# Kernel tuning notes

Hardware: AMD Instinct MI355X
Metric: run time of the kernel (lower is better)

The kernel has to match this reference:

```python
import jax, jax.numpy as jnp
import numpy as np

LN_EPS = 1e-5


def setup_inputs() -> dict:
    key = jax.random.key(0)
    k1, k2, k3, k4, k5, k6 = jax.random.split(key, 6)
    B, S, P = 4, 4096, 16          # batch, seq_len, max_n_bytes
    LR, D = 256, 1024              # lowrank_dim, embedding_dim
    # byte ids in [-1, 255]; -1 marks missing bytes
    bytes_ids = jax.random.randint(k1, (B, S, P), -1, 256)
    byte_table = jax.random.normal(k2, (256, LR), dtype=jnp.float32) * 0.02
    pos_emb = jax.random.normal(k3, (P, LR, LR), dtype=jnp.float32)
    W_up = jax.random.normal(k4, (D, LR), dtype=jnp.float32) * 0.02
    b_up = jnp.zeros((D,), dtype=jnp.float32)
    ln_gamma = jnp.ones((D,), dtype=jnp.float32)
    ln_beta = jnp.zeros((D,), dtype=jnp.float32)
    return {
        "bytes_ids": bytes_ids,
        "byte_table": byte_table,
        "pos_emb": pos_emb,
        "W_up": W_up,
        "b_up": b_up,
        "ln_gamma": ln_gamma,
        "ln_beta": ln_beta,
    }


def reference(bytes_ids, byte_table, pos_emb, W_up, b_up, ln_gamma, ln_beta):
    # bytes_ids: [B, S, P] int, -1 => missing byte
    missing = bytes_ids == -1                             # [B,S,P]
    ids = jnp.where(missing, 0, bytes_ids)
    be = byte_table[ids]                                  # [B,S,P,LR] gather
    # per-position small matmul: pos_emb[p] applied to each byte embedding
    emb = jnp.einsum('pij,bspi->bspj', pos_emb, be)       # [B,S,P,LR]
    emb = jnp.where(missing[..., None], 0.0, emb)         # mask missing bytes
    emb = emb.sum(axis=-2)                                # [B,S,LR]
    x = emb @ W_up.T + b_up                               # [B,S,D]
    # layernorm
    mu = x.mean(axis=-1, keepdims=True)
    var = jnp.mean(jnp.square(x - mu), axis=-1, keepdims=True)
    return (x - mu) * jax.lax.rsqrt(var + LN_EPS) * ln_gamma + ln_beta
```

## Files before the change

kernel.cpp:

```cpp
#include <hip/hip_runtime.h>
#include <stdint.h>

#define PP     16
#define LRDIM  256
#define DDIM   1024
#define LN_EPS 1e-5f

typedef __attribute__((ext_vector_type(8))) short  short8;
typedef __attribute__((ext_vector_type(4))) float  f32x4;

__device__ __forceinline__ uint32_t bf16_rne(float f) {
    uint32_t u = __builtin_bit_cast(uint32_t, f);
    return (u + 0x7fffu + ((u >> 16) & 1u)) >> 16;
}
__device__ __forceinline__ float bf_lo(uint32_t u) {
    return __builtin_bit_cast(float, u << 16);
}
__device__ __forceinline__ float bf_hi(uint32_t u) {
    return __builtin_bit_cast(float, u & 0xffff0000u);
}

__global__ __launch_bounds__(256) void k_prep(const float* __restrict__ bt,
                                              const float* __restrict__ pe,
                                              const float* __restrict__ W,
                                              unsigned short* __restrict__ t2b,
                                              uint4* __restrict__ wb) {
    if (blockIdx.x < 512) {
        const int p  = blockIdx.x >> 5;
        const int c0 = (blockIdx.x & 31) << 3;
        const int j  = threadIdx.x;
        const float* pep = pe + (size_t)p * LRDIM * LRDIM;
        float a[8];
#pragma unroll
        for (int r = 0; r < 8; ++r) a[r] = 0.f;
#pragma unroll 4
        for (int i = 0; i < LRDIM; ++i) {
            const float v = pep[i * LRDIM + j];
#pragma unroll
            for (int r = 0; r < 8; ++r)
                a[r] = fmaf(v, bt[(c0 + r) * LRDIM + i], a[r]);
        }
#pragma unroll
        for (int r = 0; r < 8; ++r)
            t2b[(size_t)((p << 8) + c0 + r) * LRDIM + j] =
                (unsigned short)bf16_rne(a[r]);
    } else {
        const int gt  = (blockIdx.x - 512) * 256 + threadIdx.x;
        const int l   = gt & 63;
        const int ks  = (gt >> 6) & 7;
        const int nfg = gt >> 9;
        const int n   = nfg * 16 + (l & 15);
        const int k   = ks * 32 + (l >> 4) * 8;
        const float* src = W + (size_t)n * LRDIM + k;
        uint32_t r[4];
#pragma unroll
        for (int q = 0; q < 4; ++q) {
            const uint32_t lo = bf16_rne(src[2 * q + 0]);
            const uint32_t hi = bf16_rne(src[2 * q + 1]);
            r[q] = lo | (hi << 16);
        }
        wb[gt] = make_uint4(r[0], r[1], r[2], r[3]);
    }
}

__global__ __launch_bounds__(256) void k_gather(const int* __restrict__ ids,
                                                const unsigned short* __restrict__ t2b,
                                                uint2* __restrict__ Aq,
                                                int ntok) {
    const int wid = (blockIdx.x << 2) + (threadIdx.x >> 6);
    const int l   = threadIdx.x & 63;
    if (wid >= ntok) return;

    const int myid = (l < PP) ? ids[(size_t)wid * PP + l] : -1;

    float a0 = 0.f, a1 = 0.f, a2 = 0.f, a3 = 0.f;
#pragma unroll
    for (int p = 0; p < PP; ++p) {
        const int   id  = __shfl(myid, p);
        const float msk = (id >= 0) ? 1.f : 0.f;
        const uint2 v = *(const uint2*)(t2b +
                          ((size_t)((p << 8) + (id & 255)) << 8) + (l << 2));
        a0 = fmaf(msk, bf_lo(v.x), a0);
        a1 = fmaf(msk, bf_hi(v.x), a1);
        a2 = fmaf(msk, bf_lo(v.y), a2);
        a3 = fmaf(msk, bf_hi(v.y), a3);
    }
    uint2 pk;
    pk.x = bf16_rne(a0) | (bf16_rne(a1) << 16);
    pk.y = bf16_rne(a2) | (bf16_rne(a3) << 16);
    Aq[(size_t)wid * 64 + l] = pk;
}

__global__ __launch_bounds__(512, 4) void k_gemm(const unsigned short* __restrict__ A,
                                                 const uint4* __restrict__ wb,
                                                 const float* __restrict__ b_up,
                                                 const float* __restrict__ gamma,
                                                 const float* __restrict__ beta,
                                                 float* __restrict__ out,
                                                 int ntok) {
    __shared__ float ln_s[8][32];
    __shared__ float ln_ss[8][32];

    const int t    = threadIdx.x;
    const int w    = t >> 6;
    const int l    = t & 63;
    const int lo4  = l & 15;
    const int hi2  = l >> 4;
    const int tok0 = blockIdx.x << 5;

    f32x4 acc[2][8];
#pragma unroll
    for (int m2 = 0; m2 < 2; ++m2)
#pragma unroll
        for (int nf = 0; nf < 8; ++nf) {
            f32x4 z = {0.f, 0.f, 0.f, 0.f};
            acc[m2][nf] = z;
        }

    const unsigned short* Abase = A + ((size_t)tok0 << 8);

#pragma unroll
    for (int ks = 0; ks < 8; ++ks) {
        short8 af[2];
#pragma unroll
        for (int m2 = 0; m2 < 2; ++m2) {
            const int row = (m2 << 4) + lo4;
            af[m2] = *(const short8*)(Abase + ((size_t)row << 8) + (ks << 5) + (hi2 << 3));
        }
#pragma unroll
        for (int nf = 0; nf < 8; ++nf) {
            const int nfg = (w << 3) + nf;
            const uint4 bv = wb[(size_t)((nfg << 3) + ks) * 64 + l];
            const short8 bfr = __builtin_bit_cast(short8, bv);
            acc[0][nf] = __builtin_amdgcn_mfma_f32_16x16x32_bf16(af[0], bfr, acc[0][nf], 0, 0, 0);
            acc[1][nf] = __builtin_amdgcn_mfma_f32_16x16x32_bf16(af[1], bfr, acc[1][nf], 0, 0, 0);
        }
    }

    float s_[8], ss_[8];
#pragma unroll
    for (int q = 0; q < 8; ++q) { s_[q] = 0.f; ss_[q] = 0.f; }

#pragma unroll
    for (int nf = 0; nf < 8; ++nf) {
        const int col = (w << 7) + (nf << 4) + lo4;
        const float bu = b_up[col];
#pragma unroll
        for (int m2 = 0; m2 < 2; ++m2) {
            f32x4 v = acc[m2][nf];
            v.x += bu; v.y += bu; v.z += bu; v.w += bu;
            acc[m2][nf] = v;
            const int q0 = m2 * 4;
            s_[q0 + 0] += v.x; ss_[q0 + 0] += v.x * v.x;
            s_[q0 + 1] += v.y; ss_[q0 + 1] += v.y * v.y;
            s_[q0 + 2] += v.z; ss_[q0 + 2] += v.z * v.z;
            s_[q0 + 3] += v.w; ss_[q0 + 3] += v.w * v.w;
        }
    }
#pragma unroll
    for (int off = 1; off < 16; off <<= 1)
#pragma unroll
        for (int q = 0; q < 8; ++q) {
            s_[q]  += __shfl_xor(s_[q], off);
            ss_[q] += __shfl_xor(ss_[q], off);
        }
    if (lo4 == 0) {
#pragma unroll
        for (int q = 0; q < 8; ++q) {
            const int tl = (q >> 2) * 16 + hi2 * 4 + (q & 3);
            ln_s[w][tl]  = s_[q];
            ln_ss[w][tl] = ss_[q];
        }
    }
    __syncthreads();

    float mu_[8], inv_[8];
#pragma unroll
    for (int q = 0; q < 8; ++q) {
        const int tl = (q >> 2) * 16 + hi2 * 4 + (q & 3);
        float S = 0.f, SS = 0.f;
#pragma unroll
        for (int ww = 0; ww < 8; ++ww) { S += ln_s[ww][tl]; SS += ln_ss[ww][tl]; }
        const float mu  = S * (1.f / DDIM);
        const float var = SS * (1.f / DDIM) - mu * mu;
        mu_[q]  = mu;
        inv_[q] = rsqrtf(var + LN_EPS);
    }

#pragma unroll
    for (int nf = 0; nf < 8; ++nf) {
        const int col = (w << 7) + (nf << 4) + lo4;
        const float g  = gamma[col];
        const float bb = beta[col];
#pragma unroll
        for (int m2 = 0; m2 < 2; ++m2) {
            const f32x4 v = acc[m2][nf];
#pragma unroll
            for (int r = 0; r < 4; ++r) {
                const int q   = m2 * 4 + r;
                const int tl  = m2 * 16 + hi2 * 4 + r;
                const int tok = tok0 + tl;
                if (tok < ntok)
                    out[(size_t)tok * DDIM + col] = (v[r] - mu_[q]) * inv_[q] * g + bb;
            }
        }
    }
}

extern "C" void kernel_launch(void* const* d_in, const int* in_sizes, int n_in,
                              void* d_out, int out_size, void* d_ws, size_t ws_size,
                              hipStream_t stream) {
    const int*   ids   = (const int*)  d_in[0];
    const float* bt    = (const float*)d_in[1];
    const float* pe    = (const float*)d_in[2];
    const float* W     = (const float*)d_in[3];
    const float* b_up  = (const float*)d_in[4];
    const float* gamma = (const float*)d_in[5];
    const float* beta  = (const float*)d_in[6];
    float* out = (float*)d_out;

    const int ntok = in_sizes[0] / PP;

    char* ws = (char*)d_ws;
    unsigned short* t2b = (unsigned short*)(ws);
    uint4*          wbb = (uint4*)(ws + (2 << 20));
    unsigned short* Abf = (unsigned short*)(ws + (3 << 20));
    uint2*          Aq  = (uint2*)Abf;

    hipLaunchKernelGGL(k_prep, dim3(640), dim3(256), 0, stream, bt, pe, W, t2b, wbb);
    hipLaunchKernelGGL(k_gather, dim3((ntok + 3) / 4), dim3(256), 0, stream,
                       ids, t2b, Aq, ntok);
    hipLaunchKernelGGL(k_gemm, dim3((ntok + 31) / 32), dim3(512), 0, stream,
                       Abf, wbb, b_up, gamma, beta, out, ntok);
}
```

Baseline: 90.16 us.

## Restructure GEMM to 16-token tiles with LDS-staged A and double-buffered B

The GEMM+LayerNorm kernel now processes 16 tokens per block with 4 waves, each wave covering 256 output columns (16 MFMA tiles) instead of 32 tokens × 128 columns. The A tile is staged once into swizzled LDS to avoid bank conflicts, and the B fragments are software-pipelined with two register buffers so weight loads overlap the MFMAs. This halves A reuse per B fragment (B is reloaded per 16 tokens, so weight traffic from L2 doubles) in exchange for more blocks and latency hiding.

```diff
diff --git a/kernel.cpp b/kernel.cpp
--- a/kernel.cpp
+++ b/kernel.cpp
@@ -91,96 +91,122 @@
     Aq[(size_t)wid * 64 + l] = pk;
 }
 
-__global__ __launch_bounds__(512, 4) void k_gemm(const unsigned short* __restrict__ A,
+__global__ __launch_bounds__(256, 4) void k_gemm(const unsigned short* __restrict__ A,
                                                  const uint4* __restrict__ wb,
                                                  const float* __restrict__ b_up,
                                                  const float* __restrict__ gamma,
                                                  const float* __restrict__ beta,
                                                  float* __restrict__ out,
                                                  int ntok) {
-    __shared__ float ln_s[8][32];
-    __shared__ float ln_ss[8][32];
+    __shared__ __align__(16) unsigned char As[16 * 512];
+    __shared__ float ln_s[4][16];
+    __shared__ float ln_ss[4][16];
 
     const int t    = threadIdx.x;
     const int w    = t >> 6;
     const int l    = t & 63;
     const int lo4  = l & 15;
     const int hi2  = l >> 4;
-    const int tok0 = blockIdx.x << 5;
-
-    f32x4 acc[2][8];
-#pragma unroll
-    for (int m2 = 0; m2 < 2; ++m2)
-#pragma unroll
-        for (int nf = 0; nf < 8; ++nf) {
-            f32x4 z = {0.f, 0.f, 0.f, 0.f};
-            acc[m2][nf] = z;
-        }
-
-    const unsigned short* Abase = A + ((size_t)tok0 << 8);
+    const int tok0 = blockIdx.x << 4;
+
+    {
+        const int r = t >> 4;
+        const int c = t & 15;
+        const uint4* asrc = (const uint4*)(A + ((size_t)(tok0 + r) << 8)) + (c << 1);
+        const uint4 v0 = asrc[0];
+        const uint4 v1 = asrc[1];
+        const int sw = (r & 7) << 4;
+        *(uint4*)(As + (r << 9) + (((c << 5)     ) ^ sw)) = v0;
+        *(uint4*)(As + (r << 9) + (((c << 5) + 16) ^ sw)) = v1;
+    }
+    __syncthreads();
+
+    f32x4 acc[16];
+#pragma unroll
+    for (int nf = 0; nf < 16; ++nf) {
+        f32x4 z = {0.f, 0.f, 0.f, 0.f};
+        acc[nf] = z;
+    }
+
+    const uint4* wp = wb + ((size_t)w << 13) + l;
+    const int swz = (lo4 & 7) << 4;
+
+    uint4 bA[4], bB[4];
+#pragma unroll
+    for (int h = 0; h < 4; ++h) bA[h] = wp[h * 512];
 
 #pragma unroll
     for (int ks = 0; ks < 8; ++ks) {
-        short8 af[2];
-#pragma unroll
-        for (int m2 = 0; m2 < 2; ++m2) {
-            const int row = (m2 << 4) + lo4;
-            af[m2] = *(const short8*)(Abase + ((size_t)row << 8) + (ks << 5) + (hi2 << 3));
-        }
-#pragma unroll
-        for (int nf = 0; nf < 8; ++nf) {
-            const int nfg = (w << 3) + nf;
-            const uint4 bv = wb[(size_t)((nfg << 3) + ks) * 64 + l];
-            const short8 bfr = __builtin_bit_cast(short8, bv);
-            acc[0][nf] = __builtin_amdgcn_mfma_f32_16x16x32_bf16(af[0], bfr, acc[0][nf], 0, 0, 0);
-            acc[1][nf] = __builtin_amdgcn_mfma_f32_16x16x32_bf16(af[1], bfr, acc[1][nf], 0, 0, 0);
-        }
-    }
-
-    float s_[8], ss_[8];
-#pragma unroll
-    for (int q = 0; q < 8; ++q) { s_[q] = 0.f; ss_[q] = 0.f; }
-
-#pragma unroll
-    for (int nf = 0; nf < 8; ++nf) {
-        const int col = (w << 7) + (nf << 4) + lo4;
+        const short8 af = *(const short8*)(As + (lo4 << 9) +
+                                           (((ks << 6) + (hi2 << 4)) ^ swz));
+#pragma unroll
+        for (int g = 0; g < 4; ++g) {
+            const int gn   = (g + 1) & 3;
+            const int kn   = (g == 3) ? ks + 1 : ks;
+            const bool last = (ks == 7) && (g == 3);
+            if ((g & 1) == 0) {
+                if (!last) {
+#pragma unroll
+                    for (int h = 0; h < 4; ++h)
+                        bB[h] = wp[(gn * 4 + h) * 512 + kn * 64];
+                }
+#pragma unroll
+                for (int h = 0; h < 4; ++h)
+                    acc[g * 4 + h] = __builtin_amdgcn_mfma_f32_16x16x32_bf16(
+                        af, __builtin_bit_cast(short8, bA[h]), acc[g * 4 + h], 0, 0, 0);
+            } else {
+                if (!last) {
+#pragma unroll
+                    for (int h = 0; h < 4; ++h)
+                        bA[h] = wp[(gn * 4 + h) * 512 + kn * 64];
+                }
+#pragma unroll
+                for (int h = 0; h < 4; ++h)
+                    acc[g * 4 + h] = __builtin_amdgcn_mfma_f32_16x16x32_bf16(
+                        af, __builtin_bit_cast(short8, bB[h]), acc[g * 4 + h], 0, 0, 0);
+            }
+        }
+    }
+
+    float s_[4], ss_[4];
+#pragma unroll
+    for (int q = 0; q < 4; ++q) { s_[q] = 0.f; ss_[q] = 0.f; }
+
+#pragma unroll
+    for (int nf = 0; nf < 16; ++nf) {
+        const int col = (w << 8) + (nf << 4) + lo4;
         const float bu = b_up[col];
-#pragma unroll
-        for (int m2 = 0; m2 < 2; ++m2) {
-            f32x4 v = acc[m2][nf];
-            v.x += bu; v.y += bu; v.z += bu; v.w += bu;
-            acc[m2][nf] = v;
-            const int q0 = m2 * 4;
-            s_[q0 + 0] += v.x; ss_[q0 + 0] += v.x * v.x;
-            s_[q0 + 1] += v.y; ss_[q0 + 1] += v.y * v.y;
-            s_[q0 + 2] += v.z; ss_[q0 + 2] += v.z * v.z;
-            s_[q0 + 3] += v.w; ss_[q0 + 3] += v.w * v.w;
-        }
+        f32x4 v = acc[nf];
+        v.x += bu; v.y += bu; v.z += bu; v.w += bu;
+        acc[nf] = v;
+        s_[0] += v.x; ss_[0] += v.x * v.x;
+        s_[1] += v.y; ss_[1] += v.y * v.y;
+        s_[2] += v.z; ss_[2] += v.z * v.z;
+        s_[3] += v.w; ss_[3] += v.w * v.w;
     }
 #pragma unroll
     for (int off = 1; off < 16; off <<= 1)
 #pragma unroll
-        for (int q = 0; q < 8; ++q) {
+        for (int q = 0; q < 4; ++q) {
             s_[q]  += __shfl_xor(s_[q], off);
             ss_[q] += __shfl_xor(ss_[q], off);
         }
     if (lo4 == 0) {
 #pragma unroll
-        for (int q = 0; q < 8; ++q) {
-            const int tl = (q >> 2) * 16 + hi2 * 4 + (q & 3);
-            ln_s[w][tl]  = s_[q];
-            ln_ss[w][tl] = ss_[q];
+        for (int q = 0; q < 4; ++q) {
+            ln_s[w][hi2 * 4 + q]  = s_[q];
+            ln_ss[w][hi2 * 4 + q] = ss_[q];
         }
     }
     __syncthreads();
 
-    float mu_[8], inv_[8];
-#pragma unroll
-    for (int q = 0; q < 8; ++q) {
-        const int tl = (q >> 2) * 16 + hi2 * 4 + (q & 3);
+    float mu_[4], inv_[4];
+#pragma unroll
+    for (int q = 0; q < 4; ++q) {
+        const int tl = hi2 * 4 + q;
         float S = 0.f, SS = 0.f;
 #pragma unroll
-        for (int ww = 0; ww < 8; ++ww) { S += ln_s[ww][tl]; SS += ln_ss[ww][tl]; }
+        for (int ww = 0; ww < 4; ++ww) { S += ln_s[ww][tl]; SS += ln_ss[ww][tl]; }
         const float mu  = S * (1.f / DDIM);
         const float var = SS * (1.f / DDIM) - mu * mu;
         mu_[q]  = mu;
@@ -188,21 +214,16 @@
     }
 
 #pragma unroll
-    for (int nf = 0; nf < 8; ++nf) {
-        const int col = (w << 7) + (nf << 4) + lo4;
+    for (int nf = 0; nf < 16; ++nf) {
+        const int col = (w << 8) + (nf << 4) + lo4;
         const float g  = gamma[col];
         const float bb = beta[col];
-#pragma unroll
-        for (int m2 = 0; m2 < 2; ++m2) {
-            const f32x4 v = acc[m2][nf];
-#pragma unroll
-            for (int r = 0; r < 4; ++r) {
-                const int q   = m2 * 4 + r;
-                const int tl  = m2 * 16 + hi2 * 4 + r;
-                const int tok = tok0 + tl;
-                if (tok < ntok)
-                    out[(size_t)tok * DDIM + col] = (v[r] - mu_[q]) * inv_[q] * g + bb;
-            }
+        const f32x4 v = acc[nf];
+#pragma unroll
+        for (int r = 0; r < 4; ++r) {
+            const int tok = tok0 + hi2 * 4 + r;
+            if (tok < ntok)
+                out[(size_t)tok * DDIM + col] = (v[r] - mu_[r]) * inv_[r] * g + bb;
         }
     }
 }
@@ -230,6 +251,6 @@
     hipLaunchKernelGGL(k_prep, dim3(640), dim3(256), 0, stream, bt, pe, W, t2b, wbb);
     hipLaunchKernelGGL(k_gather, dim3((ntok + 3) / 4), dim3(256), 0, stream,
                        ids, t2b, Aq, ntok);
-    hipLaunchKernelGGL(k_gemm, dim3((ntok + 31) / 32), dim3(512), 0, stream,
+    hipLaunchKernelGGL(k_gemm, dim3((ntok + 15) / 16), dim3(256), 0, stream,
                        Abf, wbb, b_up, gamma, beta, out, ntok);
 }
```

Result: no change. 89.33 us (-0.9%).

## Stage A tile in LDS via direct global-to-LDS loads with swizzle, prefetch B

Applied to the files above, without the earlier changes.

The gather kernel now writes A rows with an XOR swizzle. The GEMM kernel copies the block's 32-token A tile into LDS using global_load_lds and then reads the fragments from LDS at swizzled offsets, which avoids bank conflicts. The packed W layout is reordered so that ks is the outer index, and B fragments are software-prefetched in groups of four so loads overlap the MFMAs. The cost is extra LDS use, which may lower occupancy, plus a block-wide barrier.

```diff
diff --git a/kernel.cpp b/kernel.cpp
--- a/kernel.cpp
+++ b/kernel.cpp
@@ -18,6 +18,12 @@
 }
 __device__ __forceinline__ float bf_hi(uint32_t u) {
     return __builtin_bit_cast(float, u & 0xffff0000u);
+}
+
+typedef __attribute__((address_space(3))) uint32_t       lds_u32;
+typedef const __attribute__((address_space(1))) uint32_t glb_u32;
+__device__ __forceinline__ void gload_lds16(const void* g, void* l) {
+    __builtin_amdgcn_global_load_lds((glb_u32*)g, (lds_u32*)l, 16, 0, 0);
 }
 
 __global__ __launch_bounds__(256) void k_prep(const float* __restrict__ bt,
@@ -59,7 +65,7 @@
             const uint32_t hi = bf16_rne(src[2 * q + 1]);
             r[q] = lo | (hi << 16);
         }
-        wb[gt] = make_uint4(r[0], r[1], r[2], r[3]);
+        wb[((ks << 6) + nfg) * 64 + l] = make_uint4(r[0], r[1], r[2], r[3]);
     }
 }
 
@@ -88,7 +94,7 @@
     uint2 pk;
     pk.x = bf16_rne(a0) | (bf16_rne(a1) << 16);
     pk.y = bf16_rne(a2) | (bf16_rne(a3) << 16);
-    Aq[(size_t)wid * 64 + l] = pk;
+    Aq[((size_t)wid << 6) + (l ^ ((wid & 7) << 1))] = pk;
 }
 
 __global__ __launch_bounds__(512, 4) void k_gemm(const unsigned short* __restrict__ A,
@@ -98,6 +104,7 @@
                                                  const float* __restrict__ beta,
                                                  float* __restrict__ out,
                                                  int ntok) {
+    __shared__ __align__(16) unsigned char As[32 * 512];
     __shared__ float ln_s[8][32];
     __shared__ float ln_ss[8][32];
 
@@ -108,6 +115,12 @@
     const int hi2  = l >> 4;
     const int tok0 = blockIdx.x << 5;
 
+    {
+        const uint4* asrc = (const uint4*)(A + ((size_t)tok0 << 8));
+        gload_lds16(asrc + t,       As + (t << 4));
+        gload_lds16(asrc + 512 + t, As + 8192 + (t << 4));
+    }
+
     f32x4 acc[2][8];
 #pragma unroll
     for (int m2 = 0; m2 < 2; ++m2)
@@ -117,7 +130,16 @@
             acc[m2][nf] = z;
         }
 
-    const unsigned short* Abase = A + ((size_t)tok0 << 8);
+    const uint4* wpB = wb + ((size_t)(w << 9) + l);
+#define BLD(ks_, nf_) wpB[((ks_) << 12) + ((nf_) << 6)]
+
+    uint4 bP[4];
+#pragma unroll
+    for (int j = 0; j < 4; ++j) bP[j] = BLD(0, j);
+
+    __syncthreads();
+
+    const int swz = (lo4 & 7) << 4;
 
 #pragma unroll
     for (int ks = 0; ks < 8; ++ks) {
@@ -125,17 +147,29 @@
 #pragma unroll
         for (int m2 = 0; m2 < 2; ++m2) {
             const int row = (m2 << 4) + lo4;
-            af[m2] = *(const short8*)(Abase + ((size_t)row << 8) + (ks << 5) + (hi2 << 3));
-        }
-#pragma unroll
-        for (int nf = 0; nf < 8; ++nf) {
-            const int nfg = (w << 3) + nf;
-            const uint4 bv = wb[(size_t)((nfg << 3) + ks) * 64 + l];
-            const short8 bfr = __builtin_bit_cast(short8, bv);
-            acc[0][nf] = __builtin_amdgcn_mfma_f32_16x16x32_bf16(af[0], bfr, acc[0][nf], 0, 0, 0);
-            acc[1][nf] = __builtin_amdgcn_mfma_f32_16x16x32_bf16(af[1], bfr, acc[1][nf], 0, 0, 0);
-        }
-    }
+            af[m2] = *(const short8*)(As + (row << 9) +
+                                      (((ks << 6) + (hi2 << 4)) ^ swz));
+        }
+#pragma unroll
+        for (int j = 0; j < 4; ++j) {
+            const short8 bfr = __builtin_bit_cast(short8, bP[j]);
+            acc[0][j] = __builtin_amdgcn_mfma_f32_16x16x32_bf16(af[0], bfr, acc[0][j], 0, 0, 0);
+            acc[1][j] = __builtin_amdgcn_mfma_f32_16x16x32_bf16(af[1], bfr, acc[1][j], 0, 0, 0);
+        }
+#pragma unroll
+        for (int j = 0; j < 4; ++j) bP[j] = BLD(ks, 4 + j);
+#pragma unroll
+        for (int j = 0; j < 4; ++j) {
+            const short8 bfr = __builtin_bit_cast(short8, bP[j]);
+            acc[0][4 + j] = __builtin_amdgcn_mfma_f32_16x16x32_bf16(af[0], bfr, acc[0][4 + j], 0, 0, 0);
+            acc[1][4 + j] = __builtin_amdgcn_mfma_f32_16x16x32_bf16(af[1], bfr, acc[1][4 + j], 0, 0, 0);
+        }
+        if (ks < 7) {
+#pragma unroll
+            for (int j = 0; j < 4; ++j) bP[j] = BLD(ks + 1, j);
+        }
+    }
+#undef BLD
 
     float s_[8], ss_[8];
 #pragma unroll
```

Measured after the change: 85.57 us. -5.1%, faster.

## Split GEMM across 16 waves and double-buffer weight fragment loads

Applied to the files above, without the earlier changes.

The GEMM block grows from 8 to 16 waves, each owning 64 output columns instead of 128, which halves per-wave accumulators. The packed weight layout changes to ks-major so each wave's fragments for a k-step are contiguous, and B fragments are prefetched two k-steps ahead in alternating register banks so loads overlap the MFMAs. The layernorm reduction now spans 16 waves through shared memory. The trade-off is more shared-memory reduction work and more duplicated A loads, since each of the extra waves fetches the same A rows.

```diff
diff --git a/kernel.cpp b/kernel.cpp
--- a/kernel.cpp
+++ b/kernel.cpp
@@ -59,7 +59,7 @@
             const uint32_t hi = bf16_rne(src[2 * q + 1]);
             r[q] = lo | (hi << 16);
         }
-        wb[gt] = make_uint4(r[0], r[1], r[2], r[3]);
+        wb[((ks << 6) + nfg) * 64 + l] = make_uint4(r[0], r[1], r[2], r[3]);
     }
 }
 
@@ -88,18 +88,18 @@
     uint2 pk;
     pk.x = bf16_rne(a0) | (bf16_rne(a1) << 16);
     pk.y = bf16_rne(a2) | (bf16_rne(a3) << 16);
-    Aq[(size_t)wid * 64 + l] = pk;
-}
-
-__global__ __launch_bounds__(512, 4) void k_gemm(const unsigned short* __restrict__ A,
-                                                 const uint4* __restrict__ wb,
-                                                 const float* __restrict__ b_up,
-                                                 const float* __restrict__ gamma,
-                                                 const float* __restrict__ beta,
-                                                 float* __restrict__ out,
-                                                 int ntok) {
-    __shared__ float ln_s[8][32];
-    __shared__ float ln_ss[8][32];
+    Aq[((size_t)wid << 6) + l] = pk;
+}
+
+__global__ __launch_bounds__(1024) void k_gemm(const unsigned short* __restrict__ A,
+                                               const uint4* __restrict__ wb,
+                                               const float* __restrict__ b_up,
+                                               const float* __restrict__ gamma,
+                                               const float* __restrict__ beta,
+                                               float* __restrict__ out,
+                                               int ntok) {
+    __shared__ float ln_s[16][32];
+    __shared__ float ln_ss[16][32];
 
     const int t    = threadIdx.x;
     const int w    = t >> 6;
@@ -108,42 +108,55 @@
     const int hi2  = l >> 4;
     const int tok0 = blockIdx.x << 5;
 
-    f32x4 acc[2][8];
+    f32x4 acc[2][4];
 #pragma unroll
     for (int m2 = 0; m2 < 2; ++m2)
 #pragma unroll
-        for (int nf = 0; nf < 8; ++nf) {
+        for (int nf = 0; nf < 4; ++nf) {
             f32x4 z = {0.f, 0.f, 0.f, 0.f};
             acc[m2][nf] = z;
         }
 
     const unsigned short* Abase = A + ((size_t)tok0 << 8);
-
-#pragma unroll
-    for (int ks = 0; ks < 8; ++ks) {
-        short8 af[2];
-#pragma unroll
-        for (int m2 = 0; m2 < 2; ++m2) {
-            const int row = (m2 << 4) + lo4;
-            af[m2] = *(const short8*)(Abase + ((size_t)row << 8) + (ks << 5) + (hi2 << 3));
-        }
-#pragma unroll
-        for (int nf = 0; nf < 8; ++nf) {
-            const int nfg = (w << 3) + nf;
-            const uint4 bv = wb[(size_t)((nfg << 3) + ks) * 64 + l];
-            const short8 bfr = __builtin_bit_cast(short8, bv);
-            acc[0][nf] = __builtin_amdgcn_mfma_f32_16x16x32_bf16(af[0], bfr, acc[0][nf], 0, 0, 0);
-            acc[1][nf] = __builtin_amdgcn_mfma_f32_16x16x32_bf16(af[1], bfr, acc[1][nf], 0, 0, 0);
-        }
-    }
+    const uint4* wpB = wb + ((size_t)(w << 8) + l);
+#define BLD(ks_, nf_) wpB[((ks_) << 12) + ((nf_) << 6)]
+
+    uint4 b0[4], b1[4];
+#pragma unroll
+    for (int j = 0; j < 4; ++j) b0[j] = BLD(0, j);
+#pragma unroll
+    for (int j = 0; j < 4; ++j) b1[j] = BLD(1, j);
+
+#define KSTEP(KS, BANK)                                                       \
+    {                                                                         \
+        const short8 af0 = *(const short8*)(Abase + (lo4 << 8) +              \
+                                            ((KS) << 5) + (hi2 << 3));        \
+        const short8 af1 = *(const short8*)(Abase + ((16 + lo4) << 8) +       \
+                                            ((KS) << 5) + (hi2 << 3));        \
+        _Pragma("unroll")                                                     \
+        for (int j = 0; j < 4; ++j) {                                         \
+            const short8 bfr = __builtin_bit_cast(short8, BANK[j]);           \
+            acc[0][j] = __builtin_amdgcn_mfma_f32_16x16x32_bf16(af0, bfr, acc[0][j], 0, 0, 0); \
+            acc[1][j] = __builtin_amdgcn_mfma_f32_16x16x32_bf16(af1, bfr, acc[1][j], 0, 0, 0); \
+        }                                                                     \
+        if ((KS) < 6) {                                                       \
+            _Pragma("unroll")                                                 \
+            for (int j = 0; j < 4; ++j) BANK[j] = BLD((KS) + 2, j);           \
+        }                                                                     \
+    }
+
+    KSTEP(0, b0) KSTEP(1, b1) KSTEP(2, b0) KSTEP(3, b1)
+    KSTEP(4, b0) KSTEP(5, b1) KSTEP(6, b0) KSTEP(7, b1)
+#undef KSTEP
+#undef BLD
 
     float s_[8], ss_[8];
 #pragma unroll
     for (int q = 0; q < 8; ++q) { s_[q] = 0.f; ss_[q] = 0.f; }
 
 #pragma unroll
-    for (int nf = 0; nf < 8; ++nf) {
-        const int col = (w << 7) + (nf << 4) + lo4;
+    for (int nf = 0; nf < 4; ++nf) {
+        const int col = (w << 6) + (nf << 4) + lo4;
         const float bu = b_up[col];
 #pragma unroll
         for (int m2 = 0; m2 < 2; ++m2) {
@@ -180,7 +193,7 @@
         const int tl = (q >> 2) * 16 + hi2 * 4 + (q & 3);
         float S = 0.f, SS = 0.f;
 #pragma unroll
-        for (int ww = 0; ww < 8; ++ww) { S += ln_s[ww][tl]; SS += ln_ss[ww][tl]; }
+        for (int ww = 0; ww < 16; ++ww) { S += ln_s[ww][tl]; SS += ln_ss[ww][tl]; }
         const float mu  = S * (1.f / DDIM);
         const float var = SS * (1.f / DDIM) - mu * mu;
         mu_[q]  = mu;
@@ -188,8 +201,8 @@
     }
 
 #pragma unroll
-    for (int nf = 0; nf < 8; ++nf) {
-        const int col = (w << 7) + (nf << 4) + lo4;
+    for (int nf = 0; nf < 4; ++nf) {
+        const int col = (w << 6) + (nf << 4) + lo4;
         const float g  = gamma[col];
         const float bb = beta[col];
 #pragma unroll
@@ -230,6 +243,6 @@
     hipLaunchKernelGGL(k_prep, dim3(640), dim3(256), 0, stream, bt, pe, W, t2b, wbb);
     hipLaunchKernelGGL(k_gather, dim3((ntok + 3) / 4), dim3(256), 0, stream,
                        ids, t2b, Aq, ntok);
-    hipLaunchKernelGGL(k_gemm, dim3((ntok + 31) / 32), dim3(512), 0, stream,
+    hipLaunchKernelGGL(k_gemm, dim3((ntok + 31) / 32), dim3(1024), 0, stream,
                        Abf, wbb, b_up, gamma, beta, out, ntok);
 }
```

Measured after the change: 155.3 us. +72.3%, slower.
